# Performance work log

Measured on AMD Instinct MI355X. Metric: run time of the kernel, lower is better.

The kernel has to match this reference:

```python
import jax, jax.numpy as jnp
import numpy as np

HEADS = 8
DIM_HEAD = 32


def setup_inputs() -> dict:
    key = jax.random.key(0)
    k1, k2, k3 = jax.random.split(key, 3)
    dim = 256
    hd = HEADS * DIM_HEAD  # 256
    x = jax.random.normal(k1, (2, dim, 16, 64, 64), dtype=jnp.float32)
    w_qkv = jax.random.normal(k2, (3 * hd, dim), dtype=jnp.float32) * (1.0 / np.sqrt(dim))
    w_out = jax.random.normal(k3, (dim, hd), dtype=jnp.float32) * (1.0 / np.sqrt(hd))
    b_out = jnp.zeros((dim,), dtype=jnp.float32)
    return {"x": x, "w_qkv": w_qkv, "w_out": w_out, "b_out": b_out}


def reference(x, w_qkv, w_out, b_out):
    b, c, f, h, w = x.shape
    n = h * w
    scale = DIM_HEAD ** (-0.5)
    # (b c f h w) -> ((b f) c (h w))
    xr = jnp.transpose(x, (0, 2, 1, 3, 4)).reshape(b * f, c, n)
    # 1x1 conv (no bias) == channel GEMM
    qkv = jnp.einsum('oc,bcn->bon', w_qkv, xr)  # (bf, 3*H*D, n)
    q, k, v = jnp.split(qkv, 3, axis=1)
    def heads(t):
        return t.reshape(b * f, HEADS, DIM_HEAD, n)
    q, k, v = heads(q), heads(k), heads(v)
    q = jax.nn.softmax(q, axis=-2) * scale   # softmax over feature dim d
    k = jax.nn.softmax(k, axis=-1)           # softmax over spatial dim n
    context = jnp.einsum('bhdn,bhen->bhde', k, v)   # (bf, H, D, D)
    out = jnp.einsum('bhde,bhdn->bhen', context, q)  # (bf, H, D, n)
    out = out.reshape(b * f, HEADS * DIM_HEAD, n)
    out = jnp.einsum('oc,bcn->bon', w_out, out) + b_out[None, :, None]
    # ((b f) c (h w)) -> (b c f h w)
    out = out.reshape(b, f, c, h, w)
    return jnp.transpose(out, (0, 2, 1, 3, 4))
```

## Files before the change

### kernel.cpp

```cpp
#include <hip/hip_runtime.h>
#include <cmath>


typedef unsigned short u16;
typedef __attribute__((ext_vector_type(4))) unsigned short u16x4;
typedef __attribute__((ext_vector_type(8))) unsigned short u16x8;
typedef __attribute__((ext_vector_type(4))) unsigned int   u32x4;
typedef __attribute__((ext_vector_type(8))) short bf16x8;
typedef __attribute__((ext_vector_type(4))) float f32x4;

#define XCH_STRIDE 65536
#define XB_STRIDE  16777216

__device__ __forceinline__ float bf2f(u16 u) {
    union { unsigned int i; float f; } w; w.i = ((unsigned int)u) << 16; return w.f;
}
__device__ __forceinline__ u16 f2bf(float f) {
    union { float f; unsigned int i; } w; w.f = f;
    return (u16)((w.i + 0x7FFFu + ((w.i >> 16) & 1u)) >> 16);
}
__device__ __forceinline__ void async16(const void* g, void* l) {
    __builtin_amdgcn_global_load_lds(
        (const __attribute__((address_space(1))) unsigned int*)g,
        (__attribute__((address_space(3))) unsigned int*)l, 16, 0, 0);
}

__global__ __launch_bounds__(256) void k_cvt_x(const float* __restrict__ x,
                                               u16* __restrict__ xbf, int fr0)
{
    const int tid = threadIdx.x;
    const int n0 = blockIdx.x * 64;
    const int c0 = blockIdx.y * 64;
    const int fl = blockIdx.z;
    const int frame = fr0 + fl, b = frame >> 4, f = frame & 15;
    const float* xb = x + (size_t)b * XB_STRIDE + (size_t)f * 4096;
    __shared__ float T[64][65];
    const int nn = tid & 63, cq = tid >> 6;
    #pragma unroll
    for (int r = 0; r < 16; ++r) {
        const int cl = r * 4 + cq;
        T[cl][nn] = xb[(size_t)(c0 + cl) * XCH_STRIDE + n0 + nn];
    }
    __syncthreads();
    const int jl = tid >> 2, c16 = (tid & 3) * 16;
    u16* dst = xbf + ((size_t)fl * 4096 + n0 + jl) * 256 + c0 + c16;
    u16x8 a, bv;
    #pragma unroll
    for (int i = 0; i < 8; ++i) a[i] = f2bf(T[c16 + i][jl]);
    #pragma unroll
    for (int i = 0; i < 8; ++i) bv[i] = f2bf(T[c16 + 8 + i][jl]);
    *(u16x8*)dst = a;
    *(u16x8*)(dst + 8) = bv;
}

__global__ __launch_bounds__(256) void k_cvt_w(const float* __restrict__ w,
                                               u16* __restrict__ wbf)
{
    const int i = (blockIdx.x * 256 + threadIdx.x) * 8;
    u16x8 o;
    #pragma unroll
    for (int j = 0; j < 8; ++j) o[j] = f2bf(w[i + j]);
    *(u16x8*)(wbf + i) = o;
}

__global__ __launch_bounds__(256) void k_qkv_mfma(const u16* __restrict__ xbf,
                                                  const u16* __restrict__ wq,
                                                  u16* __restrict__ qkv)
{
    const int tid = threadIdx.x;
    const int lane = tid & 63, wave = tid >> 6;
    const int ln = lane & 15, quad = lane >> 4;
    const int wm = wave & 1, wn = wave >> 1;

    const int chunk = gridDim.x >> 3;
    const int newid = (blockIdx.x & 7) * chunk + (blockIdx.x >> 3);
    const int o0 = (newid % 6) * 128;
    const int j0 = (newid / 6) * 128;

    __shared__ __align__(16) u16 sm[128 * 136];
    u16* As = sm;
    u16* Bs = sm + 4096;

    f32x4 acc[4][4] = {};
    const int lrow = lane >> 2;
    const int lk8 = ((lane & 3) ^ ((lrow >> 1) & 3)) * 8;
    const int sw8 = (quad ^ ((ln >> 1) & 3)) * 8;

    for (int kk = 0; kk < 256; kk += 32) {
        __syncthreads();
        #pragma unroll
        for (int p = 0; p < 2; ++p) {
            const int ch = wave * 2 + p;
            const int r = ch * 16 + lrow;
            async16(wq  + (size_t)(o0 + r) * 256 + kk + lk8, As + ch * 512);
            async16(xbf + (size_t)(j0 + r) * 256 + kk + lk8, Bs + ch * 512);
        }
        __syncthreads();
        bf16x8 af[4], bfv[4];
        #pragma unroll
        for (int mi = 0; mi < 4; ++mi)
            af[mi] = *(const bf16x8*)&As[(wm * 64 + mi * 16 + ln) * 32 + sw8];
        #pragma unroll
        for (int ni = 0; ni < 4; ++ni)
            bfv[ni] = *(const bf16x8*)&Bs[(wn * 64 + ni * 16 + ln) * 32 + sw8];
        #pragma unroll
        for (int mi = 0; mi < 4; ++mi)
            #pragma unroll
            for (int ni = 0; ni < 4; ++ni)
                acc[mi][ni] = __builtin_amdgcn_mfma_f32_16x16x32_bf16(
                    af[mi], bfv[ni], acc[mi][ni], 0, 0, 0);
    }

    __syncthreads();
    u16* outl = sm;
    #pragma unroll
    for (int mi = 0; mi < 4; ++mi)
        #pragma unroll
        for (int ni = 0; ni < 4; ++ni) {
            const int jl = wn * 64 + ni * 16 + ln;
            const int ob = wm * 64 + mi * 16 + quad * 4;
            u16x4 u;
            u[0] = f2bf(acc[mi][ni][0]); u[1] = f2bf(acc[mi][ni][1]);
            u[2] = f2bf(acc[mi][ni][2]); u[3] = f2bf(acc[mi][ni][3]);
            *(u16x4*)&outl[jl * 136 + ob] = u;
        }
    __syncthreads();

    if (o0 < 256) {
        #pragma unroll
        for (int t = 0; t < 2; ++t) {
            const int idx = t * 256 + tid;
            const int r = idx >> 2, hh = idx & 3;
            const u16* p = &outl[r * 136 + hh * 32];
            float v[32];
            float m = -1e30f;
            #pragma unroll
            for (int g = 0; g < 4; ++g) {
                u16x8 u = *(const u16x8*)(p + g * 8);
                #pragma unroll
                for (int i = 0; i < 8; ++i) {
                    v[g * 8 + i] = bf2f(u[i]);
                    m = fmaxf(m, v[g * 8 + i]);
                }
            }
            float s = 0.f;
            #pragma unroll
            for (int i = 0; i < 32; ++i) { v[i] = __expf(v[i] - m); s += v[i]; }
            const float inv = 0.17677669529663687f / s;
            u16* q = qkv + (size_t)(j0 + r) * 768 + o0 + hh * 32;
            #pragma unroll
            for (int g = 0; g < 4; ++g) {
                u16x8 ov;
                #pragma unroll
                for (int i = 0; i < 8; ++i) ov[i] = f2bf(v[g * 8 + i] * inv);
                *(u16x8*)(q + g * 8) = ov;
            }
        }
    } else {
        #pragma unroll
        for (int r = 0; r < 8; ++r) {
            const int row = r * 16 + (tid >> 4);
            const int cb = (tid & 15) * 8;
            u32x4 v = *(const u32x4*)&outl[row * 136 + cb];
            *(u32x4*)(qkv + (size_t)(j0 + row) * 768 + o0 + cb) = v;
        }
    }
}

__global__ __launch_bounds__(256) void k_kstat1(const u16* __restrict__ qkv,
                                                float* __restrict__ sp)
{
    const int js = blockIdx.x, fl = blockIdx.y;
    const int tid = threadIdx.x;
    const int s = tid >> 5, g = tid & 31;
    const u16* base = qkv + ((size_t)fl * 4096 + js * 256 + s) * 768 + 256 + g * 8;
    float m[8], sm[8];
    #pragma unroll
    for (int i = 0; i < 8; ++i) { m[i] = -1e30f; sm[i] = 0.f; }
    for (int it = 0; it < 32; ++it) {
        u16x8 u = *(const u16x8*)(base + (size_t)it * 8 * 768);
        #pragma unroll
        for (int i = 0; i < 8; ++i) {
            float v = bf2f(u[i]);
            float nm = fmaxf(m[i], v);
            sm[i] = sm[i] * __expf(m[i] - nm) + __expf(v - nm);
            m[i] = nm;
        }
    }
    __shared__ float Lm[8][256], Ls[8][256];
    #pragma unroll
    for (int i = 0; i < 8; ++i) { Lm[s][g * 8 + i] = m[i]; Ls[s][g * 8 + i] = sm[i]; }
    __syncthreads();
    const int col = tid;
    float M = -1e30f;
    #pragma unroll
    for (int k = 0; k < 8; ++k) M = fmaxf(M, Lm[k][col]);
    float S = 0.f;
    #pragma unroll
    for (int k = 0; k < 8; ++k) S += Ls[k][col] * __expf(Lm[k][col] - M);
    float* o = sp + (((size_t)fl * 16 + js) * 256 + col) * 2;
    o[0] = M; o[1] = S;
}

__global__ __launch_bounds__(256) void k_kstat2(const float* __restrict__ sp,
                                                float* __restrict__ stat)
{
    const int fl = blockIdx.x, col = threadIdx.x;
    float mv[16], sv[16];
    float M = -1e30f;
    #pragma unroll
    for (int js = 0; js < 16; ++js) {
        const float* p = sp + (((size_t)fl * 16 + js) * 256 + col) * 2;
        mv[js] = p[0]; sv[js] = p[1];
        M = fmaxf(M, mv[js]);
    }
    float S = 0.f;
    #pragma unroll
    for (int js = 0; js < 16; ++js) S += sv[js] * __expf(mv[js] - M);
    float* o = stat + ((size_t)fl * 256 + col) * 2;
    o[0] = M; o[1] = 1.0f / S;
}

__global__ __launch_bounds__(256) void k_ctx(const u16* __restrict__ qkv,
                                             const float* __restrict__ stat,
                                             float* __restrict__ P)
{
    const int js = blockIdx.x, fl = blockIdx.y;
    const int tid = threadIdx.x;
    const int ls = tid >> 5, lg = tid & 31;
    const int h = tid >> 5, dg = (tid >> 3) & 3, eg = tid & 7;
    const int d0 = dg * 8, e0 = eg * 4;

    float Mg[8];
    #pragma unroll
    for (int i = 0; i < 8; ++i) Mg[i] = stat[((size_t)fl * 256 + lg * 8 + i) * 2];

    __shared__ float expk[8][264], vbuf[8][264];
    f32x4 acc[8] = {};
    const u16* kbase = qkv + ((size_t)fl * 4096 + js * 256 + ls) * 768 + 256 + lg * 8;

    for (int ch = 0; ch < 32; ++ch) {
        const u16* kp = kbase + (size_t)ch * 8 * 768;
        u16x8 ku = *(const u16x8*)kp;
        u16x8 vu = *(const u16x8*)(kp + 256);
        __syncthreads();
        #pragma unroll
        for (int i = 0; i < 8; ++i) {
            expk[ls][lg * 8 + i] = __expf(bf2f(ku[i]) - Mg[i]);
            vbuf[ls][lg * 8 + i] = bf2f(vu[i]);
        }
        __syncthreads();
        #pragma unroll
        for (int rr = 0; rr < 8; ++rr) {
            f32x4 w0 = *(const f32x4*)&expk[rr][h * 32 + d0];
            f32x4 w1 = *(const f32x4*)&expk[rr][h * 32 + d0 + 4];
            f32x4 vv = *(const f32x4*)&vbuf[rr][h * 32 + e0];
            #pragma unroll
            for (int ei = 0; ei < 4; ++ei) {
                acc[0][ei] = fmaf(w0[0], vv[ei], acc[0][ei]);
                acc[1][ei] = fmaf(w0[1], vv[ei], acc[1][ei]);
                acc[2][ei] = fmaf(w0[2], vv[ei], acc[2][ei]);
                acc[3][ei] = fmaf(w0[3], vv[ei], acc[3][ei]);
                acc[4][ei] = fmaf(w1[0], vv[ei], acc[4][ei]);
                acc[5][ei] = fmaf(w1[1], vv[ei], acc[5][ei]);
                acc[6][ei] = fmaf(w1[2], vv[ei], acc[6][ei]);
                acc[7][ei] = fmaf(w1[3], vv[ei], acc[7][ei]);
            }
        }
    }
    float* o = P + ((size_t)fl * 16 + js) * 8192 + (h * 32 + d0) * 32 + e0;
    #pragma unroll
    for (int di = 0; di < 8; ++di) *(f32x4*)(o + di * 32) = acc[di];
}

__global__ __launch_bounds__(256) void k_w2fold(const float* __restrict__ P,
                                                const float* __restrict__ stat,
                                                const float* __restrict__ w_out,
                                                u16* __restrict__ w2)
{
    const int h = blockIdx.x, fl = blockIdx.y;
    const int tid = threadIdx.x;
    __shared__ float Cs[32 * 33];

    const float* p0 = P + (size_t)fl * 16 * 8192 + h * 1024 + tid * 4;
    f32x4 sum = {0.f, 0.f, 0.f, 0.f};
    #pragma unroll
    for (int js = 0; js < 16; ++js) {
        f32x4 v = *(const f32x4*)(p0 + (size_t)js * 8192);
        sum[0] += v[0]; sum[1] += v[1]; sum[2] += v[2]; sum[3] += v[3];
    }
    const int d = tid >> 3, e4 = (tid & 7) * 4;
    const float inv = stat[((size_t)fl * 256 + h * 32 + d) * 2 + 1];
    Cs[d * 33 + e4 + 0] = sum[0] * inv;
    Cs[d * 33 + e4 + 1] = sum[1] * inv;
    Cs[d * 33 + e4 + 2] = sum[2] * inv;
    Cs[d * 33 + e4 + 3] = sum[3] * inv;
    __syncthreads();

    const int o = tid;
    float a2[32];
    #pragma unroll
    for (int dd = 0; dd < 32; ++dd) a2[dd] = 0.f;
    for (int e = 0; e < 32; ++e) {
        const float wv = w_out[(size_t)o * 256 + h * 32 + e];
        #pragma unroll
        for (int dd = 0; dd < 32; ++dd) a2[dd] = fmaf(wv, Cs[dd * 33 + e], a2[dd]);
    }
    u16* wp = w2 + (size_t)fl * 65536 + (size_t)o * 256 + h * 32;
    #pragma unroll
    for (int g = 0; g < 4; ++g) {
        u16x8 ov;
        #pragma unroll
        for (int i = 0; i < 8; ++i) ov[i] = f2bf(a2[g * 8 + i]);
        *(u16x8*)(wp + g * 8) = ov;
    }
}

__global__ __launch_bounds__(256) void k_out_mfma(const u16* __restrict__ qkv,
                                                  const u16* __restrict__ w2,
                                                  const float* __restrict__ b_out,
                                                  float* __restrict__ out, int fr0)
{
    const int tid = threadIdx.x;
    const int lane = tid & 63, wave = tid >> 6;
    const int ln = lane & 15, quad = lane >> 4;
    const int wm = wave & 1, wn = wave >> 1;

    const int chunk = gridDim.x >> 3;
    const int newid = (blockIdx.x & 7) * chunk + (blockIdx.x >> 3);
    const int o0 = (newid & 1) * 128;
    const int j0 = (newid >> 1) * 128;

    const int fl = j0 >> 12;
    const int frame = fr0 + fl, b = frame >> 4, f = frame & 15;
    const int nb = j0 & 4095;
    const u16* w2f = w2 + (size_t)fl * 65536;

    __shared__ __align__(16) u16 sm[8192];
    u16* As = sm;
    u16* Bs = sm + 4096;

    f32x4 acc[4][4] = {};
    const int lrow = lane >> 2;
    const int lk8 = ((lane & 3) ^ ((lrow >> 1) & 3)) * 8;
    const int sw8 = (quad ^ ((ln >> 1) & 3)) * 8;

    for (int kk = 0; kk < 256; kk += 32) {
        __syncthreads();
        #pragma unroll
        for (int p = 0; p < 2; ++p) {
            const int ch = wave * 2 + p;
            const int r = ch * 16 + lrow;
            async16(qkv + (size_t)(j0 + r) * 768 + kk + lk8, As + ch * 512);
            async16(w2f + (size_t)(o0 + r) * 256 + kk + lk8, Bs + ch * 512);
        }
        __syncthreads();
        bf16x8 af[4], bfv[4];
        #pragma unroll
        for (int mi = 0; mi < 4; ++mi)
            af[mi] = *(const bf16x8*)&As[(wm * 64 + mi * 16 + ln) * 32 + sw8];
        #pragma unroll
        for (int ni = 0; ni < 4; ++ni)
            bfv[ni] = *(const bf16x8*)&Bs[(wn * 64 + ni * 16 + ln) * 32 + sw8];
        #pragma unroll
        for (int mi = 0; mi < 4; ++mi)
            #pragma unroll
            for (int ni = 0; ni < 4; ++ni)
                acc[mi][ni] = __builtin_amdgcn_mfma_f32_16x16x32_bf16(
                    af[mi], bfv[ni], acc[mi][ni], 0, 0, 0);
    }

    float* obase = out + (size_t)b * XB_STRIDE + (size_t)f * 4096;
    #pragma unroll
    for (int ni = 0; ni < 4; ++ni) {
        const int o = o0 + wn * 64 + ni * 16 + ln;
        const float bias = b_out[o];
        #pragma unroll
        for (int mi = 0; mi < 4; ++mi) {
            const int jn = nb + wm * 64 + mi * 16 + quad * 4;
            f32x4 v = acc[mi][ni];
            v[0] += bias; v[1] += bias; v[2] += bias; v[3] += bias;
            *(f32x4*)(obase + (size_t)o * XCH_STRIDE + jn) = v;
        }
    }
}

extern "C" void kernel_launch(void* const* d_in, const int* in_sizes, int n_in,
                              void* d_out, int out_size, void* d_ws, size_t ws_size,
                              hipStream_t stream)
{
    const float* x     = (const float*)d_in[0];
    const float* w_qkv = (const float*)d_in[1];
    const float* w_out = (const float*)d_in[2];
    const float* b_out = (const float*)d_in[3];
    float* out = (float*)d_out;

    const size_t per_frame = (size_t)4096 * 256 * 2 + (size_t)4096 * 768 * 2
                           + 65536 * 2 + 16 * 512 * 4 + 512 * 4 + 16 * 8192 * 4;
    const size_t wq_bytes = 768 * 256 * 2;
    int CF = 32;
    while (CF > 1 && (size_t)CF * per_frame + wq_bytes > ws_size) CF >>= 1;

    u16* wq_bf  = (u16*)d_ws;
    u16* xbf    = wq_bf + 768 * 256;
    u16* qkv    = xbf + (size_t)CF * 4096 * 256;
    u16* w2     = qkv + (size_t)CF * 4096 * 768;
    float* sp   = (float*)(w2 + (size_t)CF * 65536);
    float* stat = sp + (size_t)CF * 16 * 256 * 2;
    float* P    = stat + (size_t)CF * 256 * 2;

    k_cvt_w<<<96, 256, 0, stream>>>(w_qkv, wq_bf);
    for (int fr0 = 0; fr0 < 32; fr0 += CF) {
        k_cvt_x   <<<dim3(64, 4, CF), 256, 0, stream>>>(x, xbf, fr0);
        k_qkv_mfma<<<CF * 32 * 6, 256, 0, stream>>>(xbf, wq_bf, qkv);
        k_kstat1  <<<dim3(16, CF), 256, 0, stream>>>(qkv, sp);
        k_kstat2  <<<CF, 256, 0, stream>>>(sp, stat);
        k_ctx     <<<dim3(16, CF), 256, 0, stream>>>(qkv, stat, P);
        k_w2fold  <<<dim3(8, CF), 256, 0, stream>>>(P, stat, w_out, w2);
        k_out_mfma<<<CF * 32 * 2, 256, 0, stream>>>(qkv, w2, b_out, out, fr0);
    }
}
```

Before: 482.6 us.

## Double-buffer LDS tiles in QKV and output GEMM kernels

Both MFMA GEMM kernels now ping-pong between two LDS buffers. The next K-slice is loaded asynchronously while MFMAs run on the current slice, with one vmcnt wait and barrier per iteration instead of two syncthreads around each load. This is meant to hide global-to-LDS latency behind compute. The cost is a doubled LDS footprint in the output kernel, which may reduce occupancy. There is also a possible hazard: a buffer is overwritten while other waves may still be reading it, guarded only by the end-of-iteration barrier.

Result: no change. 476.7 us (-1.2%).

```diff
diff --git a/kernel.cpp b/kernel.cpp
--- a/kernel.cpp
+++ b/kernel.cpp
@@ -78,24 +78,40 @@
     const int j0 = (newid / 6) * 128;
 
     __shared__ __align__(16) u16 sm[128 * 136];
-    u16* As = sm;
-    u16* Bs = sm + 4096;
 
     f32x4 acc[4][4] = {};
     const int lrow = lane >> 2;
     const int lk8 = ((lane & 3) ^ ((lrow >> 1) & 3)) * 8;
     const int sw8 = (quad ^ ((ln >> 1) & 3)) * 8;
 
-    for (int kk = 0; kk < 256; kk += 32) {
-        __syncthreads();
-        #pragma unroll
-        for (int p = 0; p < 2; ++p) {
-            const int ch = wave * 2 + p;
-            const int r = ch * 16 + lrow;
-            async16(wq  + (size_t)(o0 + r) * 256 + kk + lk8, As + ch * 512);
-            async16(xbf + (size_t)(j0 + r) * 256 + kk + lk8, Bs + ch * 512);
-        }
-        __syncthreads();
+    const u16* gA = wq  + (size_t)o0 * 256;
+    const u16* gB = xbf + (size_t)j0 * 256;
+    const int r0 = wave * 32 + lrow;
+
+    {
+        u16* A = sm;      u16* B = sm + 4096;
+        async16(gA + (size_t)r0 * 256 + lk8,          A + (wave*2) * 512);
+        async16(gB + (size_t)r0 * 256 + lk8,          B + (wave*2) * 512);
+        async16(gA + (size_t)(r0+16) * 256 + lk8,     A + (wave*2+1) * 512);
+        async16(gB + (size_t)(r0+16) * 256 + lk8,     B + (wave*2+1) * 512);
+    }
+    asm volatile("s_waitcnt vmcnt(0)" ::: "memory");
+    __builtin_amdgcn_s_barrier();
+
+    #pragma unroll
+    for (int t = 0; t < 8; ++t) {
+        const int cur = t & 1;
+        if (t < 7) {
+            u16* A = sm + (cur ^ 1) * 8192;
+            u16* B = A + 4096;
+            const int kk = (t + 1) * 32;
+            async16(gA + (size_t)r0 * 256 + kk + lk8,      A + (wave*2) * 512);
+            async16(gB + (size_t)r0 * 256 + kk + lk8,      B + (wave*2) * 512);
+            async16(gA + (size_t)(r0+16) * 256 + kk + lk8, A + (wave*2+1) * 512);
+            async16(gB + (size_t)(r0+16) * 256 + kk + lk8, B + (wave*2+1) * 512);
+        }
+        const u16* As = sm + cur * 8192;
+        const u16* Bs = As + 4096;
         bf16x8 af[4], bfv[4];
         #pragma unroll
         for (int mi = 0; mi < 4; ++mi)
@@ -109,6 +125,10 @@
             for (int ni = 0; ni < 4; ++ni)
                 acc[mi][ni] = __builtin_amdgcn_mfma_f32_16x16x32_bf16(
                     af[mi], bfv[ni], acc[mi][ni], 0, 0, 0);
+        if (t < 7) {
+            asm volatile("s_waitcnt vmcnt(0)" ::: "memory");
+            __builtin_amdgcn_s_barrier();
+        }
     }
 
     __syncthreads();
@@ -336,25 +356,41 @@
     const int nb = j0 & 4095;
     const u16* w2f = w2 + (size_t)fl * 65536;
 
-    __shared__ __align__(16) u16 sm[8192];
-    u16* As = sm;
-    u16* Bs = sm + 4096;
+    __shared__ __align__(16) u16 sm[16384];
 
     f32x4 acc[4][4] = {};
     const int lrow = lane >> 2;
     const int lk8 = ((lane & 3) ^ ((lrow >> 1) & 3)) * 8;
     const int sw8 = (quad ^ ((ln >> 1) & 3)) * 8;
 
-    for (int kk = 0; kk < 256; kk += 32) {
-        __syncthreads();
-        #pragma unroll
-        for (int p = 0; p < 2; ++p) {
-            const int ch = wave * 2 + p;
-            const int r = ch * 16 + lrow;
-            async16(qkv + (size_t)(j0 + r) * 768 + kk + lk8, As + ch * 512);
-            async16(w2f + (size_t)(o0 + r) * 256 + kk + lk8, Bs + ch * 512);
-        }
-        __syncthreads();
+    const u16* gA = qkv + (size_t)j0 * 768;
+    const u16* gB = w2f + (size_t)o0 * 256;
+    const int r0 = wave * 32 + lrow;
+
+    {
+        u16* A = sm;      u16* B = sm + 4096;
+        async16(gA + (size_t)r0 * 768 + lk8,          A + (wave*2) * 512);
+        async16(gB + (size_t)r0 * 256 + lk8,          B + (wave*2) * 512);
+        async16(gA + (size_t)(r0+16) * 768 + lk8,     A + (wave*2+1) * 512);
+        async16(gB + (size_t)(r0+16) * 256 + lk8,     B + (wave*2+1) * 512);
+    }
+    asm volatile("s_waitcnt vmcnt(0)" ::: "memory");
+    __builtin_amdgcn_s_barrier();
+
+    #pragma unroll
+    for (int t = 0; t < 8; ++t) {
+        const int cur = t & 1;
+        if (t < 7) {
+            u16* A = sm + (cur ^ 1) * 8192;
+            u16* B = A + 4096;
+            const int kk = (t + 1) * 32;
+            async16(gA + (size_t)r0 * 768 + kk + lk8,      A + (wave*2) * 512);
+            async16(gB + (size_t)r0 * 256 + kk + lk8,      B + (wave*2) * 512);
+            async16(gA + (size_t)(r0+16) * 768 + kk + lk8, A + (wave*2+1) * 512);
+            async16(gB + (size_t)(r0+16) * 256 + kk + lk8, B + (wave*2+1) * 512);
+        }
+        const u16* As = sm + cur * 8192;
+        const u16* Bs = As + 4096;
         bf16x8 af[4], bfv[4];
         #pragma unroll
         for (int mi = 0; mi < 4; ++mi)
@@ -368,6 +404,10 @@
             for (int ni = 0; ni < 4; ++ni)
                 acc[mi][ni] = __builtin_amdgcn_mfma_f32_16x16x32_bf16(
                     af[mi], bfv[ni], acc[mi][ni], 0, 0, 0);
+        if (t < 7) {
+            asm volatile("s_waitcnt vmcnt(0)" ::: "memory");
+            __builtin_amdgcn_s_barrier();
+        }
     }
 
     float* obase = out + (size_t)b * XB_STRIDE + (size_t)f * 4096;
```

## Triple-buffer activation tiles and load weights directly to registers in QKV/out GEMMs

Applied to the files above, without the earlier changes.

Both MFMA GEMM kernels now stage only the activation operand through LDS, using a three-slot ring buffer with async global-to-LDS loads issued two k-steps ahead. The weight operand is loaded straight from global into registers and double-buffered one step ahead. Raw s_waitcnt vmcnt plus s_barrier replace the paired __syncthreads so loads overlap MFMA work and LDS traffic is halved. The hand-counted vmcnt values are fragile: they must match the exact number of outstanding loads, and the weight fragments are read from global without LDS sharing, so the four waves read them redundantly.

Measured after the change: 518.2 us. 1.07x slower.

```diff
diff --git a/kernel.cpp b/kernel.cpp
--- a/kernel.cpp
+++ b/kernel.cpp
@@ -78,28 +78,43 @@
     const int j0 = (newid / 6) * 128;
 
     __shared__ __align__(16) u16 sm[128 * 136];
-    u16* As = sm;
-    u16* Bs = sm + 4096;
 
     f32x4 acc[4][4] = {};
     const int lrow = lane >> 2;
     const int lk8 = ((lane & 3) ^ ((lrow >> 1) & 3)) * 8;
     const int sw8 = (quad ^ ((ln >> 1) & 3)) * 8;
 
-    for (int kk = 0; kk < 256; kk += 32) {
-        __syncthreads();
-        #pragma unroll
-        for (int p = 0; p < 2; ++p) {
-            const int ch = wave * 2 + p;
-            const int r = ch * 16 + lrow;
-            async16(wq  + (size_t)(o0 + r) * 256 + kk + lk8, As + ch * 512);
-            async16(xbf + (size_t)(j0 + r) * 256 + kk + lk8, Bs + ch * 512);
-        }
-        __syncthreads();
-        bf16x8 af[4], bfv[4];
-        #pragma unroll
-        for (int mi = 0; mi < 4; ++mi)
-            af[mi] = *(const bf16x8*)&As[(wm * 64 + mi * 16 + ln) * 32 + sw8];
+    const u16* gB = xbf + (size_t)j0 * 256;
+    const int r0 = wave * 32 + lrow;
+    const u16* gA0 = wq + (size_t)(o0 + wm * 64 + ln) * 256 + quad * 8;
+
+    bf16x8 afr[2][4];
+
+    async16(gB + (size_t)r0 * 256 + lk8,        sm + (wave*2) * 512);
+    async16(gB + (size_t)(r0+16) * 256 + lk8,   sm + (wave*2+1) * 512);
+    #pragma unroll
+    for (int mi = 0; mi < 4; ++mi)
+        afr[0][mi] = *(const bf16x8*)(gA0 + mi * 16 * 256);
+    async16(gB + (size_t)r0 * 256 + 32 + lk8,      sm + 4096 + (wave*2) * 512);
+    async16(gB + (size_t)(r0+16) * 256 + 32 + lk8, sm + 4096 + (wave*2+1) * 512);
+    asm volatile("s_waitcnt vmcnt(2)\n\ts_barrier" ::: "memory");
+
+    #pragma unroll
+    for (int t = 0; t < 8; ++t) {
+        const u16* Bs = sm + (t % 3) * 4096;
+        if (t < 6) {
+            u16* Bn = sm + ((t + 2) % 3) * 4096;
+            const int kk2 = (t + 2) * 32;
+            async16(gB + (size_t)r0 * 256 + kk2 + lk8,      Bn + (wave*2) * 512);
+            async16(gB + (size_t)(r0+16) * 256 + kk2 + lk8, Bn + (wave*2+1) * 512);
+        }
+        if (t < 7) {
+            const int kk1 = (t + 1) * 32;
+            #pragma unroll
+            for (int mi = 0; mi < 4; ++mi)
+                afr[(t + 1) & 1][mi] = *(const bf16x8*)(gA0 + mi * 16 * 256 + kk1);
+        }
+        bf16x8 bfv[4];
         #pragma unroll
         for (int ni = 0; ni < 4; ++ni)
             bfv[ni] = *(const bf16x8*)&Bs[(wn * 64 + ni * 16 + ln) * 32 + sw8];
@@ -108,7 +123,9 @@
             #pragma unroll
             for (int ni = 0; ni < 4; ++ni)
                 acc[mi][ni] = __builtin_amdgcn_mfma_f32_16x16x32_bf16(
-                    af[mi], bfv[ni], acc[mi][ni], 0, 0, 0);
+                    afr[t & 1][mi], bfv[ni], acc[mi][ni], 0, 0, 0);
+        if (t < 6)       asm volatile("s_waitcnt vmcnt(6)\n\ts_barrier" ::: "memory");
+        else if (t == 6) asm volatile("s_waitcnt vmcnt(4)\n\ts_barrier" ::: "memory");
     }
 
     __syncthreads();
@@ -336,38 +353,55 @@
     const int nb = j0 & 4095;
     const u16* w2f = w2 + (size_t)fl * 65536;
 
-    __shared__ __align__(16) u16 sm[8192];
-    u16* As = sm;
-    u16* Bs = sm + 4096;
+    __shared__ __align__(16) u16 sm[12288];
 
     f32x4 acc[4][4] = {};
     const int lrow = lane >> 2;
     const int lk8 = ((lane & 3) ^ ((lrow >> 1) & 3)) * 8;
     const int sw8 = (quad ^ ((ln >> 1) & 3)) * 8;
 
-    for (int kk = 0; kk < 256; kk += 32) {
-        __syncthreads();
-        #pragma unroll
-        for (int p = 0; p < 2; ++p) {
-            const int ch = wave * 2 + p;
-            const int r = ch * 16 + lrow;
-            async16(qkv + (size_t)(j0 + r) * 768 + kk + lk8, As + ch * 512);
-            async16(w2f + (size_t)(o0 + r) * 256 + kk + lk8, Bs + ch * 512);
-        }
-        __syncthreads();
-        bf16x8 af[4], bfv[4];
+    const u16* gA = qkv + (size_t)j0 * 768;
+    const int r0 = wave * 32 + lrow;
+    const u16* gB0 = w2f + (size_t)(o0 + wn * 64 + ln) * 256 + quad * 8;
+
+    bf16x8 bfr[2][4];
+
+    async16(gA + (size_t)r0 * 768 + lk8,        sm + (wave*2) * 512);
+    async16(gA + (size_t)(r0+16) * 768 + lk8,   sm + (wave*2+1) * 512);
+    #pragma unroll
+    for (int ni = 0; ni < 4; ++ni)
+        bfr[0][ni] = *(const bf16x8*)(gB0 + ni * 16 * 256);
+    async16(gA + (size_t)r0 * 768 + 32 + lk8,      sm + 4096 + (wave*2) * 512);
+    async16(gA + (size_t)(r0+16) * 768 + 32 + lk8, sm + 4096 + (wave*2+1) * 512);
+    asm volatile("s_waitcnt vmcnt(2)\n\ts_barrier" ::: "memory");
+
+    #pragma unroll
+    for (int t = 0; t < 8; ++t) {
+        const u16* As = sm + (t % 3) * 4096;
+        if (t < 6) {
+            u16* An = sm + ((t + 2) % 3) * 4096;
+            const int kk2 = (t + 2) * 32;
+            async16(gA + (size_t)r0 * 768 + kk2 + lk8,      An + (wave*2) * 512);
+            async16(gA + (size_t)(r0+16) * 768 + kk2 + lk8, An + (wave*2+1) * 512);
+        }
+        if (t < 7) {
+            const int kk1 = (t + 1) * 32;
+            #pragma unroll
+            for (int ni = 0; ni < 4; ++ni)
+                bfr[(t + 1) & 1][ni] = *(const bf16x8*)(gB0 + ni * 16 * 256 + kk1);
+        }
+        bf16x8 af[4];
         #pragma unroll
         for (int mi = 0; mi < 4; ++mi)
             af[mi] = *(const bf16x8*)&As[(wm * 64 + mi * 16 + ln) * 32 + sw8];
         #pragma unroll
-        for (int ni = 0; ni < 4; ++ni)
-            bfv[ni] = *(const bf16x8*)&Bs[(wn * 64 + ni * 16 + ln) * 32 + sw8];
-        #pragma unroll
         for (int mi = 0; mi < 4; ++mi)
             #pragma unroll
             for (int ni = 0; ni < 4; ++ni)
                 acc[mi][ni] = __builtin_amdgcn_mfma_f32_16x16x32_bf16(
-                    af[mi], bfv[ni], acc[mi][ni], 0, 0, 0);
+                    af[mi], bfr[t & 1][ni], acc[mi][ni], 0, 0, 0);
+        if (t < 6)       asm volatile("s_waitcnt vmcnt(6)\n\ts_barrier" ::: "memory");
+        else if (t == 6) asm volatile("s_waitcnt vmcnt(4)\n\ts_barrier" ::: "memory");
     }
 
     float* obase = out + (size_t)b * XB_STRIDE + (size_t)f * 4096;
```
